# Optimization experiments

Hardware: AMD Instinct MI355X
Metric: run time of the kernel (lower is better)

## Reference

```python
import jax, jax.numpy as jnp
import numpy as np

B, S, E, H = 2, 2048, 1024, 16
D = E // H  # head_dim = 64
SCALE = D ** -0.5


def setup_inputs() -> dict:
    key = jax.random.key(0)
    ks = jax.random.split(key, 5)
    std = E ** -0.5
    return {
        "x": jax.random.normal(ks[0], (B, S, E), dtype=jnp.float32),
        "wq": jax.random.normal(ks[1], (E, E), dtype=jnp.float32) * std,
        "wk": jax.random.normal(ks[2], (E, E), dtype=jnp.float32) * std,
        "wv": jax.random.normal(ks[3], (E, E), dtype=jnp.float32) * std,
        "wo": jax.random.normal(ks[4], (E, E), dtype=jnp.float32) * std,
    }


def reference(x, wq, wk, wv, wo):
    b, s, e = x.shape
    # nn.Linear(bias=False): y = x @ W.T; then split heads -> [B,H,S,D]
    def heads(w):
        return jnp.einsum('bse,fe->bsf', x, w).reshape(b, s, H, D).transpose(0, 2, 1, 3)
    q, k, v = heads(wq), heads(wk), heads(wv)
    attn = jnp.einsum('bhqd,bhkd->bhqk', q, k) * SCALE  # [B,H,S,S]
    attn = jax.nn.softmax(attn, axis=-1)
    out = jnp.einsum('bhqk,bhkd->bhqd', attn, v)        # [B,H,S,D]
    out = out.transpose(0, 2, 1, 3).reshape(b, s, e)
    return jnp.einsum('bse,fe->bsf', out, wo)
```

## Files before the change

kernel.cpp:

```cpp
#include <hip/hip_runtime.h>
#include <stdint.h>

typedef unsigned short ushort_t;
typedef __bf16 bfx8 __attribute__((ext_vector_type(8), may_alias));
typedef __bf16 bfx2 __attribute__((ext_vector_type(2), may_alias));
typedef unsigned short usx8 __attribute__((ext_vector_type(8), may_alias));
typedef unsigned int uix2 __attribute__((ext_vector_type(2), may_alias));
typedef unsigned int uix4 __attribute__((ext_vector_type(4), may_alias));
typedef float f32x2 __attribute__((ext_vector_type(2)));
typedef float f32x4 __attribute__((ext_vector_type(4)));
typedef float f32x4m __attribute__((ext_vector_type(4), may_alias));
typedef float f32x16 __attribute__((ext_vector_type(16)));

#define BB 2
#define SS 2048
#define EE 1024
#define HH 16
#define DD 64
#define MM (BB * SS)
#define XN ((size_t)MM * EE)
#define WN ((size_t)EE * EE)
#define QSCALE 0.18033688011112042f

__device__ __forceinline__ unsigned short f2bf(float f) {
  unsigned int u = __builtin_bit_cast(unsigned int, f);
  u += 0x7fffu + ((u >> 16) & 1u);
  return (unsigned short)(u >> 16);
}

__device__ __forceinline__ usx8 cvt8(const float* p) {
  f32x4m a = *(const f32x4m*)p;
  f32x4m b = *(const f32x4m*)(p + 4);
  usx8 r;
  r[0] = f2bf(a[0]); r[1] = f2bf(a[1]); r[2] = f2bf(a[2]); r[3] = f2bf(a[3]);
  r[4] = f2bf(b[0]); r[5] = f2bf(b[1]); r[6] = f2bf(b[2]); r[7] = f2bf(b[3]);
  return r;
}

__device__ __forceinline__ unsigned int pk2(float lo, float hi) {
  bfx2 t;
  t[0] = (__bf16)lo;
  t[1] = (__bf16)hi;
  return __builtin_bit_cast(unsigned int, t);
}

__device__ __forceinline__ void gl_lds16(const ushort_t* g, ushort_t* l) {
  __builtin_amdgcn_global_load_lds(
      (const __attribute__((address_space(1))) unsigned int*)g,
      (__attribute__((address_space(3))) unsigned int*)l, 16, 0, 0);
}

__global__ __launch_bounds__(256)
void cvt_qkv(const float* __restrict__ x, const float* __restrict__ wq,
             const float* __restrict__ wk, const float* __restrict__ wv,
             ushort_t* __restrict__ dst) {
  size_t i8 = ((size_t)blockIdx.x * 256 + threadIdx.x) * 8;
  const float* s;
  size_t off;
  if (i8 < XN)               { s = x;  off = i8; }
  else if (i8 < XN + WN)     { s = wq; off = i8 - XN; }
  else if (i8 < XN + 2 * WN) { s = wk; off = i8 - XN - WN; }
  else                       { s = wv; off = i8 - XN - 2 * WN; }
  *(usx8*)(dst + i8) = cvt8(s + off);
}

__global__ __launch_bounds__(256)
void cvt_one(const float* __restrict__ s, ushort_t* __restrict__ dst) {
  size_t i8 = ((size_t)blockIdx.x * 256 + threadIdx.x) * 8;
  *(usx8*)(dst + i8) = cvt8(s + i8);
}

__global__ __launch_bounds__(256)
void gemm_qkv(const ushort_t* __restrict__ xb,
              const ushort_t* __restrict__ wqb, const ushort_t* __restrict__ wkb,
              const ushort_t* __restrict__ wvb,
              ushort_t* __restrict__ Qb, ushort_t* __restrict__ Kb,
              ushort_t* __restrict__ Vtb) {
  __shared__ ushort_t As[128 * 32];
  __shared__ ushort_t Bs[128 * 32];

  const int bid = blockIdx.x;
  const ushort_t *A, *W;
  ushort_t* C;
  int bx, by, N;
  float scale = 1.0f;
  if (bid < 512) {
    int t = bid & 255;
    bx = t & 7;  by = t >> 3;
    A = xb;  N = EE;
    if (bid < 256) { W = wqb; C = Qb; scale = QSCALE; }
    else           { W = wkb; C = Kb; }
  } else {
    int t = bid - 512;
    bx = t & 31; by = t >> 5;
    A = wvb; W = xb; C = Vtb; N = MM;
  }
  const int K = EE;

  const int tid = threadIdx.x;
  const int lane = tid & 63;
  const int w = tid >> 6;
  const int l15 = lane & 15, l16 = lane >> 4;
  const int m0 = by * 128;
  const int n0 = bx * 128;
  const int wr = w >> 1, wc = w & 1;

  f32x4 acc[4][4];
#pragma unroll
  for (int i = 0; i < 4; ++i)
#pragma unroll
    for (int j = 0; j < 4; ++j)
#pragma unroll
      for (int r = 0; r < 4; ++r) acc[i][j][r] = 0.0f;

  for (int k0 = 0; k0 < K; k0 += 32) {
#pragma unroll
    for (int q = 0; q < 2; ++q) {
      int c = w * 128 + q * 64 + lane;
      int row = c >> 2, col = c & 3;
      gl_lds16(A + (size_t)(m0 + row) * K + k0 + col * 8,
               As + (size_t)(w * 128 + q * 64) * 8);
      gl_lds16(W + (size_t)(n0 + row) * K + k0 + col * 8,
               Bs + (size_t)(w * 128 + q * 64) * 8);
    }
    __syncthreads();

    bfx8 af[4], bfr[4];
#pragma unroll
    for (int i = 0; i < 4; ++i) {
      int mr = wr * 64 + i * 16 + l15;
      af[i] = *(const bfx8*)(As + mr * 32 + l16 * 8);
      int nr = wc * 64 + i * 16 + l15;
      bfr[i] = *(const bfx8*)(Bs + nr * 32 + l16 * 8);
    }
#pragma unroll
    for (int i = 0; i < 4; ++i)
#pragma unroll
      for (int j = 0; j < 4; ++j)
        acc[i][j] = __builtin_amdgcn_mfma_f32_16x16x32_bf16(af[i], bfr[j],
                                                            acc[i][j], 0, 0, 0);
    __syncthreads();
  }

#pragma unroll
  for (int i = 0; i < 4; ++i) {
    int mr = m0 + wr * 64 + i * 16 + l16 * 4;
#pragma unroll
    for (int j = 0; j < 4; ++j) {
      int nc = n0 + wc * 64 + j * 16 + l15;
#pragma unroll
      for (int r = 0; r < 4; ++r)
        C[(size_t)(mr + r) * N + nc] = f2bf(acc[i][j][r] * scale);
    }
  }
}

__global__ __launch_bounds__(256)
void gemm_o(const ushort_t* __restrict__ A, const ushort_t* __restrict__ W,
            float* __restrict__ C, int M, int N, int K) {
  __shared__ ushort_t As[128 * 32];
  __shared__ ushort_t Bs[128 * 32];

  const int tid = threadIdx.x;
  const int lane = tid & 63;
  const int w = tid >> 6;
  const int l15 = lane & 15, l16 = lane >> 4;
  const int m0 = blockIdx.y * 128;
  const int n0 = blockIdx.x * 128;
  const int wr = w >> 1, wc = w & 1;

  f32x4 acc[4][4];
#pragma unroll
  for (int i = 0; i < 4; ++i)
#pragma unroll
    for (int j = 0; j < 4; ++j)
#pragma unroll
      for (int r = 0; r < 4; ++r) acc[i][j][r] = 0.0f;

  for (int k0 = 0; k0 < K; k0 += 32) {
#pragma unroll
    for (int q = 0; q < 2; ++q) {
      int c = w * 128 + q * 64 + lane;
      int row = c >> 2, col = c & 3;
      gl_lds16(A + (size_t)(m0 + row) * K + k0 + col * 8,
               As + (size_t)(w * 128 + q * 64) * 8);
      gl_lds16(W + (size_t)(n0 + row) * K + k0 + col * 8,
               Bs + (size_t)(w * 128 + q * 64) * 8);
    }
    __syncthreads();

    bfx8 af[4], bfr[4];
#pragma unroll
    for (int i = 0; i < 4; ++i) {
      int mr = wr * 64 + i * 16 + l15;
      af[i] = *(const bfx8*)(As + mr * 32 + l16 * 8);
      int nr = wc * 64 + i * 16 + l15;
      bfr[i] = *(const bfx8*)(Bs + nr * 32 + l16 * 8);
    }
#pragma unroll
    for (int i = 0; i < 4; ++i)
#pragma unroll
      for (int j = 0; j < 4; ++j)
        acc[i][j] = __builtin_amdgcn_mfma_f32_16x16x32_bf16(af[i], bfr[j],
                                                            acc[i][j], 0, 0, 0);
    __syncthreads();
  }

#pragma unroll
  for (int i = 0; i < 4; ++i) {
    int mr = m0 + wr * 64 + i * 16 + l16 * 4;
#pragma unroll
    for (int j = 0; j < 4; ++j) {
      int nc = n0 + wc * 64 + j * 16 + l15;
#pragma unroll
      for (int r = 0; r < 4; ++r)
        C[(size_t)(mr + r) * N + nc] = acc[i][j][r];
    }
  }
}

__global__ __launch_bounds__(64, 2)
void attn_fwd(const ushort_t* Q, const ushort_t* __restrict__ Kg,
              const ushort_t* __restrict__ Vt_g, ushort_t* AO) {
  __shared__ ushort_t Ks[64 * 72];
  __shared__ ushort_t Vs[64 * 72];

  const int lane = threadIdx.x;
  const int l31 = lane & 31, hi = lane >> 5;
  const int n = blockIdx.x;
  const int xcd = n & 7, rr = n >> 3;
  const int g = xcd * 4 + (rr >> 6);
  const int qt = rr & 63;
  const int h = g & 15, b = g >> 4;
  const int q0 = qt * 32;

  const ushort_t* kbase = Kg + (size_t)b * SS * EE + h * DD;
  const ushort_t* vbase = Vt_g + (size_t)h * DD * MM + (size_t)b * SS;

  bfx8 bq[4];
#pragma unroll
  for (int t = 0; t < 4; ++t)
    bq[t] = *(const bfx8*)(Q + (size_t)(b * SS + q0 + l31) * EE + h * DD +
                           t * 16 + hi * 8);

  f32x16 o0, o1;
#pragma unroll
  for (int r = 0; r < 16; ++r) { o0[r] = 0.0f; o1[r] = 0.0f; }
  f32x2 ls2;
  ls2[0] = 0.0f; ls2[1] = 0.0f;

  const int srow = lane >> 3, scol = lane & 7;

  usx8 kreg[8], vreg[8];
#pragma unroll
  for (int i = 0; i < 8; ++i) {
    kreg[i] = *(const usx8*)(kbase + (size_t)(srow + 8 * i) * EE + scol * 8);
    vreg[i] = *(const usx8*)(vbase + (size_t)(srow + 8 * i) * MM + scol * 8);
  }

  for (int kt = 0; kt < SS; kt += 64) {
#pragma unroll
    for (int i = 0; i < 8; ++i) {
      *(usx8*)(Ks + (srow + 8 * i) * 72 + scol * 8) = kreg[i];
      *(usx8*)(Vs + (srow + 8 * i) * 72 + scol * 8) = vreg[i];
    }
    if (kt + 64 < SS) {
#pragma unroll
      for (int i = 0; i < 8; ++i) {
        kreg[i] = *(const usx8*)(kbase + (size_t)(kt + 64 + srow + 8 * i) * EE +
                                 scol * 8);
        vreg[i] = *(const usx8*)(vbase + (size_t)(srow + 8 * i) * MM + kt + 64 +
                                 scol * 8);
      }
    }

    f32x16 pa, pb;
#pragma unroll
    for (int r = 0; r < 16; ++r) { pa[r] = 0.0f; pb[r] = 0.0f; }
    __builtin_amdgcn_s_setprio(1);
#pragma unroll
    for (int t = 0; t < 4; ++t) {
      bfx8 ak0 = *(const bfx8*)(Ks + l31 * 72 + t * 16 + hi * 8);
      bfx8 ak1 = *(const bfx8*)(Ks + (32 + l31) * 72 + t * 16 + hi * 8);
      pa = __builtin_amdgcn_mfma_f32_32x32x16_bf16(ak0, bq[t], pa, 0, 0, 0);
      pb = __builtin_amdgcn_mfma_f32_32x32x16_bf16(ak1, bq[t], pb, 0, 0, 0);
    }
    __builtin_amdgcn_s_setprio(0);

#pragma unroll
    for (int r = 0; r < 16; ++r) {
      pa[r] = __builtin_exp2f(pa[r]);
      pb[r] = __builtin_exp2f(pb[r]);
    }
#pragma unroll
    for (int s = 0; s < 8; ++s) {
      f32x2 ta, tb;
      ta[0] = pa[2 * s]; ta[1] = pa[2 * s + 1];
      tb[0] = pb[2 * s]; tb[1] = pb[2 * s + 1];
      ls2 += ta + tb;
    }

    unsigned int dwA[8], dwB[8];
#pragma unroll
    for (int s = 0; s < 8; ++s) {
      dwA[s] = pk2(pa[2 * s], pa[2 * s + 1]);
      dwB[s] = pk2(pb[2 * s], pb[2 * s + 1]);
    }
    bfx8 fd[4];
#pragma unroll
    for (int g2 = 0; g2 < 2; ++g2) {
      auto sA = __builtin_amdgcn_permlane32_swap(dwA[4 * g2 + 0],
                                                 dwA[4 * g2 + 2], false, false);
      auto sB = __builtin_amdgcn_permlane32_swap(dwA[4 * g2 + 1],
                                                 dwA[4 * g2 + 3], false, false);
      uix4 f;
      f[0] = sA[0]; f[1] = sB[0]; f[2] = sA[1]; f[3] = sB[1];
      fd[g2] = __builtin_bit_cast(bfx8, f);
      auto tA = __builtin_amdgcn_permlane32_swap(dwB[4 * g2 + 0],
                                                 dwB[4 * g2 + 2], false, false);
      auto tB = __builtin_amdgcn_permlane32_swap(dwB[4 * g2 + 1],
                                                 dwB[4 * g2 + 3], false, false);
      uix4 f2;
      f2[0] = tA[0]; f2[1] = tB[0]; f2[2] = tA[1]; f2[3] = tB[1];
      fd[2 + g2] = __builtin_bit_cast(bfx8, f2);
    }

    __builtin_amdgcn_s_setprio(1);
#pragma unroll
    for (int kk = 0; kk < 4; ++kk) {
      bfx8 av0 = *(const bfx8*)(Vs + l31 * 72 + kk * 16 + hi * 8);
      bfx8 av1 = *(const bfx8*)(Vs + (32 + l31) * 72 + kk * 16 + hi * 8);
      o0 = __builtin_amdgcn_mfma_f32_32x32x16_bf16(av0, fd[kk], o0, 0, 0, 0);
      o1 = __builtin_amdgcn_mfma_f32_32x32x16_bf16(av1, fd[kk], o1, 0, 0, 0);
    }
    __builtin_amdgcn_s_setprio(0);
  }

  float lsum = ls2[0] + ls2[1];
  lsum += __shfl_xor(lsum, 32);
  float inv = 1.0f / lsum;

  ushort_t* orow = AO + (size_t)(b * SS + q0 + l31) * EE + h * DD;
#pragma unroll
  for (int g2 = 0; g2 < 4; ++g2) {
    uix2 s0, s1;
    s0[0] = pk2(o0[4 * g2 + 0] * inv, o0[4 * g2 + 1] * inv);
    s0[1] = pk2(o0[4 * g2 + 2] * inv, o0[4 * g2 + 3] * inv);
    *(uix2*)(orow + 8 * g2 + 4 * hi) = s0;
    s1[0] = pk2(o1[4 * g2 + 0] * inv, o1[4 * g2 + 1] * inv);
    s1[1] = pk2(o1[4 * g2 + 2] * inv, o1[4 * g2 + 3] * inv);
    *(uix2*)(orow + 32 + 8 * g2 + 4 * hi) = s1;
  }
}

extern "C" void kernel_launch(void* const* d_in, const int* in_sizes, int n_in,
                              void* d_out, int out_size, void* d_ws, size_t ws_size,
                              hipStream_t stream) {
  const float* x  = (const float*)d_in[0];
  const float* wq = (const float*)d_in[1];
  const float* wk = (const float*)d_in[2];
  const float* wv = (const float*)d_in[3];
  const float* wo = (const float*)d_in[4];
  float* out = (float*)d_out;

  ushort_t* Qb  = (ushort_t*)d_ws;
  ushort_t* Kb  = Qb + XN;
  ushort_t* Vtb = Kb + XN;
  ushort_t* Ab  = Qb;
  ushort_t* S    = (ushort_t*)d_out;
  ushort_t* xb   = S;
  ushort_t* wqb  = S + XN;
  ushort_t* wkb  = S + XN + WN;
  ushort_t* wvb  = S + XN + 2 * WN;
  ushort_t* wob  = Kb;

  dim3 blk(256);
  cvt_qkv<<<dim3((unsigned)((XN + 3 * WN) / (256 * 8))), blk, 0, stream>>>(
      x, wq, wk, wv, S);
  gemm_qkv<<<dim3(768), blk, 0, stream>>>(xb, wqb, wkb, wvb, Qb, Kb, Vtb);
  attn_fwd<<<dim3(2048), dim3(64), 0, stream>>>(Qb, Kb, Vtb, Ab);
  cvt_one<<<dim3((unsigned)(WN / (256 * 8))), blk, 0, stream>>>(wo, wob);
  gemm_o<<<dim3(EE / 128, MM / 128), blk, 0, stream>>>(
      Ab, wob, out, MM, EE, EE);
}
```

Baseline: 212.7 us.

## Split attention key range across two waves per block with LDS reduction

Each attention block now runs two wavefronts, and each wave processes half of the key sequence using 32-key tiles and its own private K/V LDS region. At the end, the partial output accumulators and row sums are combined through shared memory by the second wave, which then normalizes and writes the result. The aim is more waves in flight per query tile, giving better latency hiding and CU occupancy without changing the grid size. The cost is an extra LDS reduction, a block barrier, and smaller MFMA tiles per iteration. Softmax still uses exp2 with no max subtraction, so combining partial sums needs no rescaling.

```diff
diff --git a/kernel.cpp b/kernel.cpp
--- a/kernel.cpp
+++ b/kernel.cpp
@@ -219,13 +219,14 @@
   }
 }
 
-__global__ __launch_bounds__(64, 2)
+__global__ __launch_bounds__(128, 4)
 void attn_fwd(const ushort_t* Q, const ushort_t* __restrict__ Kg,
               const ushort_t* __restrict__ Vt_g, ushort_t* AO) {
-  __shared__ ushort_t Ks[64 * 72];
-  __shared__ ushort_t Vs[64 * 72];
-
-  const int lane = threadIdx.x;
+  __shared__ ushort_t KV[2 * 4608];
+
+  const int tid = threadIdx.x;
+  const int lane = tid & 63;
+  const int w = tid >> 6;
   const int l31 = lane & 31, hi = lane >> 5;
   const int n = blockIdx.x;
   const int xcd = n & 7, rr = n >> 3;
@@ -234,6 +235,10 @@
   const int h = g & 15, b = g >> 4;
   const int q0 = qt * 32;
 
+  ushort_t* Ks = KV + w * 4608;
+  ushort_t* Vs = Ks + 2304;
+  const int kOff = w * (SS / 2);
+
   const ushort_t* kbase = Kg + (size_t)b * SS * EE + h * DD;
   const ushort_t* vbase = Vt_g + (size_t)h * DD * MM + (size_t)b * SS;
 
@@ -249,87 +254,73 @@
   f32x2 ls2;
   ls2[0] = 0.0f; ls2[1] = 0.0f;
 
-  const int srow = lane >> 3, scol = lane & 7;
-
-  usx8 kreg[8], vreg[8];
-#pragma unroll
-  for (int i = 0; i < 8; ++i) {
-    kreg[i] = *(const usx8*)(kbase + (size_t)(srow + 8 * i) * EE + scol * 8);
-    vreg[i] = *(const usx8*)(vbase + (size_t)(srow + 8 * i) * MM + scol * 8);
-  }
-
-  for (int kt = 0; kt < SS; kt += 64) {
-#pragma unroll
-    for (int i = 0; i < 8; ++i) {
-      *(usx8*)(Ks + (srow + 8 * i) * 72 + scol * 8) = kreg[i];
-      *(usx8*)(Vs + (srow + 8 * i) * 72 + scol * 8) = vreg[i];
-    }
-    if (kt + 64 < SS) {
-#pragma unroll
-      for (int i = 0; i < 8; ++i) {
-        kreg[i] = *(const usx8*)(kbase + (size_t)(kt + 64 + srow + 8 * i) * EE +
-                                 scol * 8);
-        vreg[i] = *(const usx8*)(vbase + (size_t)(srow + 8 * i) * MM + kt + 64 +
-                                 scol * 8);
+  const int kr = lane >> 3, kc = lane & 7;
+  const int vr = lane >> 2, vc = lane & 3;
+
+  usx8 kreg[4], vreg[4];
+#pragma unroll
+  for (int i = 0; i < 4; ++i) {
+    kreg[i] = *(const usx8*)(kbase + (size_t)(kOff + kr + 8 * i) * EE + kc * 8);
+    vreg[i] = *(const usx8*)(vbase + (size_t)(vr + 16 * i) * MM + kOff + vc * 8);
+  }
+
+  for (int kt = 0; kt < SS / 2; kt += 32) {
+#pragma unroll
+    for (int i = 0; i < 4; ++i) {
+      *(usx8*)(Ks + (kr + 8 * i) * 72 + kc * 8) = kreg[i];
+      *(usx8*)(Vs + (vr + 16 * i) * 36 + vc * 8) = vreg[i];
+    }
+    if (kt + 32 < SS / 2) {
+#pragma unroll
+      for (int i = 0; i < 4; ++i) {
+        kreg[i] = *(const usx8*)(kbase +
+                                 (size_t)(kOff + kt + 32 + kr + 8 * i) * EE +
+                                 kc * 8);
+        vreg[i] = *(const usx8*)(vbase + (size_t)(vr + 16 * i) * MM + kOff +
+                                 kt + 32 + vc * 8);
       }
     }
 
-    f32x16 pa, pb;
-#pragma unroll
-    for (int r = 0; r < 16; ++r) { pa[r] = 0.0f; pb[r] = 0.0f; }
+    f32x16 pa;
+#pragma unroll
+    for (int r = 0; r < 16; ++r) pa[r] = 0.0f;
     __builtin_amdgcn_s_setprio(1);
 #pragma unroll
     for (int t = 0; t < 4; ++t) {
-      bfx8 ak0 = *(const bfx8*)(Ks + l31 * 72 + t * 16 + hi * 8);
-      bfx8 ak1 = *(const bfx8*)(Ks + (32 + l31) * 72 + t * 16 + hi * 8);
-      pa = __builtin_amdgcn_mfma_f32_32x32x16_bf16(ak0, bq[t], pa, 0, 0, 0);
-      pb = __builtin_amdgcn_mfma_f32_32x32x16_bf16(ak1, bq[t], pb, 0, 0, 0);
+      bfx8 ak = *(const bfx8*)(Ks + l31 * 72 + t * 16 + hi * 8);
+      pa = __builtin_amdgcn_mfma_f32_32x32x16_bf16(ak, bq[t], pa, 0, 0, 0);
     }
     __builtin_amdgcn_s_setprio(0);
 
 #pragma unroll
-    for (int r = 0; r < 16; ++r) {
-      pa[r] = __builtin_exp2f(pa[r]);
-      pb[r] = __builtin_exp2f(pb[r]);
-    }
+    for (int r = 0; r < 16; ++r) pa[r] = __builtin_exp2f(pa[r]);
 #pragma unroll
     for (int s = 0; s < 8; ++s) {
-      f32x2 ta, tb;
+      f32x2 ta;
       ta[0] = pa[2 * s]; ta[1] = pa[2 * s + 1];
-      tb[0] = pb[2 * s]; tb[1] = pb[2 * s + 1];
-      ls2 += ta + tb;
-    }
-
-    unsigned int dwA[8], dwB[8];
-#pragma unroll
-    for (int s = 0; s < 8; ++s) {
-      dwA[s] = pk2(pa[2 * s], pa[2 * s + 1]);
-      dwB[s] = pk2(pb[2 * s], pb[2 * s + 1]);
-    }
-    bfx8 fd[4];
+      ls2 += ta;
+    }
+
+    unsigned int dw[8];
+#pragma unroll
+    for (int s = 0; s < 8; ++s) dw[s] = pk2(pa[2 * s], pa[2 * s + 1]);
+    bfx8 fd[2];
 #pragma unroll
     for (int g2 = 0; g2 < 2; ++g2) {
-      auto sA = __builtin_amdgcn_permlane32_swap(dwA[4 * g2 + 0],
-                                                 dwA[4 * g2 + 2], false, false);
-      auto sB = __builtin_amdgcn_permlane32_swap(dwA[4 * g2 + 1],
-                                                 dwA[4 * g2 + 3], false, false);
+      auto sA = __builtin_amdgcn_permlane32_swap(dw[4 * g2 + 0], dw[4 * g2 + 2],
+                                                 false, false);
+      auto sB = __builtin_amdgcn_permlane32_swap(dw[4 * g2 + 1], dw[4 * g2 + 3],
+                                                 false, false);
       uix4 f;
       f[0] = sA[0]; f[1] = sB[0]; f[2] = sA[1]; f[3] = sB[1];
       fd[g2] = __builtin_bit_cast(bfx8, f);
-      auto tA = __builtin_amdgcn_permlane32_swap(dwB[4 * g2 + 0],
-                                                 dwB[4 * g2 + 2], false, false);
-      auto tB = __builtin_amdgcn_permlane32_swap(dwB[4 * g2 + 1],
-                                                 dwB[4 * g2 + 3], false, false);
-      uix4 f2;
-      f2[0] = tA[0]; f2[1] = tB[0]; f2[2] = tA[1]; f2[3] = tB[1];
-      fd[2 + g2] = __builtin_bit_cast(bfx8, f2);
     }
 
     __builtin_amdgcn_s_setprio(1);
 #pragma unroll
-    for (int kk = 0; kk < 4; ++kk) {
-      bfx8 av0 = *(const bfx8*)(Vs + l31 * 72 + kk * 16 + hi * 8);
-      bfx8 av1 = *(const bfx8*)(Vs + (32 + l31) * 72 + kk * 16 + hi * 8);
+    for (int kk = 0; kk < 2; ++kk) {
+      bfx8 av0 = *(const bfx8*)(Vs + l31 * 36 + kk * 16 + hi * 8);
+      bfx8 av1 = *(const bfx8*)(Vs + (32 + l31) * 36 + kk * 16 + hi * 8);
       o0 = __builtin_amdgcn_mfma_f32_32x32x16_bf16(av0, fd[kk], o0, 0, 0, 0);
       o1 = __builtin_amdgcn_mfma_f32_32x32x16_bf16(av1, fd[kk], o1, 0, 0, 0);
     }
@@ -337,19 +328,38 @@
   }
 
   float lsum = ls2[0] + ls2[1];
-  lsum += __shfl_xor(lsum, 32);
-  float inv = 1.0f / lsum;
-
-  ushort_t* orow = AO + (size_t)(b * SS + q0 + l31) * EE + h * DD;
-#pragma unroll
-  for (int g2 = 0; g2 < 4; ++g2) {
-    uix2 s0, s1;
-    s0[0] = pk2(o0[4 * g2 + 0] * inv, o0[4 * g2 + 1] * inv);
-    s0[1] = pk2(o0[4 * g2 + 2] * inv, o0[4 * g2 + 3] * inv);
-    *(uix2*)(orow + 8 * g2 + 4 * hi) = s0;
-    s1[0] = pk2(o1[4 * g2 + 0] * inv, o1[4 * g2 + 1] * inv);
-    s1[1] = pk2(o1[4 * g2 + 2] * inv, o1[4 * g2 + 3] * inv);
-    *(uix2*)(orow + 32 + 8 * g2 + 4 * hi) = s1;
+
+  float* mbuf = (float*)KV;
+  if (w == 0) {
+#pragma unroll
+    for (int r = 0; r < 16; ++r) {
+      mbuf[lane * 33 + r] = o0[r];
+      mbuf[lane * 33 + 16 + r] = o1[r];
+    }
+    mbuf[lane * 33 + 32] = lsum;
+  }
+  __syncthreads();
+  if (w == 1) {
+#pragma unroll
+    for (int r = 0; r < 16; ++r) {
+      o0[r] += mbuf[lane * 33 + r];
+      o1[r] += mbuf[lane * 33 + 16 + r];
+    }
+    lsum += mbuf[lane * 33 + 32];
+    lsum += __shfl_xor(lsum, 32);
+    float inv = 1.0f / lsum;
+
+    ushort_t* orow = AO + (size_t)(b * SS + q0 + l31) * EE + h * DD;
+#pragma unroll
+    for (int g2 = 0; g2 < 4; ++g2) {
+      uix2 s0, s1;
+      s0[0] = pk2(o0[4 * g2 + 0] * inv, o0[4 * g2 + 1] * inv);
+      s0[1] = pk2(o0[4 * g2 + 2] * inv, o0[4 * g2 + 3] * inv);
+      *(uix2*)(orow + 8 * g2 + 4 * hi) = s0;
+      s1[0] = pk2(o1[4 * g2 + 0] * inv, o1[4 * g2 + 1] * inv);
+      s1[1] = pk2(o1[4 * g2 + 2] * inv, o1[4 * g2 + 3] * inv);
+      *(uix2*)(orow + 32 + 8 * g2 + 4 * hi) = s1;
+    }
   }
 }
 
@@ -378,7 +388,7 @@
   cvt_qkv<<<dim3((unsigned)((XN + 3 * WN) / (256 * 8))), blk, 0, stream>>>(
       x, wq, wk, wv, S);
   gemm_qkv<<<dim3(768), blk, 0, stream>>>(xb, wqb, wkb, wvb, Qb, Kb, Vtb);
-  attn_fwd<<<dim3(2048), dim3(64), 0, stream>>>(Qb, Kb, Vtb, Ab);
+  attn_fwd<<<dim3(2048), dim3(128), 0, stream>>>(Qb, Kb, Vtb, Ab);
   cvt_one<<<dim3((unsigned)(WN / (256 * 8))), blk, 0, stream>>>(wo, wob);
   gemm_o<<<dim3(EE / 128, MM / 128), blk, 0, stream>>>(
       Ab, wob, out, MM, EE, EE);
```

New measurement: 277.0 us. 1.3x slower.
